# Optimization experiments

Measured on AMD Instinct MI355X. Metric: run time of the kernel, lower is better.

The kernel has to match this reference:

```python
import jax, jax.numpy as jnp
import numpy as np

K = 3
CHUNK = 1000  # query chunk size for KNN distance tiles
EPS = 1e-8
GRID = 256.0  # coordinate extent (coords / stride in the original)


def _knn3(queries, refs):
    """Brute-force KNN (K=3, squared L2) computed in chunks to bound memory.
    queries: [Q,3], refs: [M,3] -> (dist [Q,3], idx [Q,3] int32)."""
    ref_sq = jnp.sum(refs * refs, axis=-1)  # [M]

    def chunk_fn(q):  # q: [CHUNK,3]
        d = jnp.sum(q * q, -1)[:, None] - 2.0 * (q @ refs.T) + ref_sq[None, :]
        d = jnp.maximum(d, 0.0)  # guard tiny negatives from cancellation
        neg_d, idx = jax.lax.top_k(-d, K)
        return -neg_d, idx

    Q = queries.shape[0]
    qs = queries.reshape(Q // CHUNK, CHUNK, 3)
    dists, idxs = jax.lax.map(chunk_fn, qs)
    return dists.reshape(Q, K), idxs.reshape(Q, K)


def setup_inputs() -> dict:
    key = jax.random.key(0)
    k1, k2, k3, k4 = jax.random.split(key, 4)
    N1, N2, C = 20000, 20000, 8
    xyz1 = jax.random.uniform(k1, (N1, 3), dtype=jnp.float32) * GRID
    point1 = jax.random.normal(k2, (N1, C), dtype=jnp.float32)
    xyz2 = jax.random.uniform(k3, (N2, 3), dtype=jnp.float32) * GRID
    motion = jax.random.normal(k4, (N2, C, 3), dtype=jnp.float32)
    return {"xyz1": xyz1, "point1": point1, "xyz2": xyz2, "motion": motion}


def reference(xyz1, point1, xyz2, motion):
    # Motion-compensated inter prediction tail of inter_prediction.forward:
    # per-channel warp, KNN(K=3) into frame 1, inverse-distance interpolation.
    N2, C, _ = motion.shape
    # xyz2_ = xyz2.unsqueeze(2) + motion -> [N2*C, 3]
    xyz2_ = (xyz2[:, None, :] + motion).reshape(N2 * C, 3)
    dist, idx = _knn3(xyz2_, xyz1)                 # [N2*C,3]
    dist = dist + EPS
    dist = dist.reshape(N2, C, K)
    idx = idx.reshape(N2, C, K)
    weights = 1.0 / dist
    weights = weights / jnp.maximum(weights.sum(axis=2, keepdims=True), 3.0)
    # knn_point1[n,c,k] = point1[idx[n,c,k], c]  (per-channel gather)
    pt = point1.T                                   # [C, N1]
    knn_point1 = pt[jnp.arange(C)[None, :, None], idx]  # [N2,C,3]
    predicted_point2 = (weights * knn_point1).sum(axis=2)  # [N2,C]
    return predicted_point2
```

## Files before the change

### kernel.cpp

```cpp
#include <hip/hip_runtime.h>
#include <math.h>

#define KNN_EPS 1e-8f
#define GH 16.0f
#define GC 16
#define NCELLS (GC * GC * GC)
#define MARGIN 1.0f
#define CAP 384
#define CAPR 64
#define CAPQ 192


__device__ __forceinline__ int cell_coord(float v) {
    int c = (int)floorf(v * (1.0f / GH));
    return min(max(c, 0), GC - 1);
}

__global__ void fused_scatter_kernel(
    const float* __restrict__ xyz1, int n1,
    const float* __restrict__ xyz2,
    const float* __restrict__ motion, int n2, int C,
    int* __restrict__ counts, int* __restrict__ qcounts,
    float4* __restrict__ rbuck, float4* __restrict__ qbuck,
    float4* __restrict__ refspill, int* __restrict__ rsn,
    float4* __restrict__ qspill, int* __restrict__ qsn)
{
#pragma clang fp contract(off)
    int i = blockIdx.x * blockDim.x + threadIdx.x;
    if (i < n1) {
        float x = xyz1[3 * i + 0];
        float y = xyz1[3 * i + 1];
        float z = xyz1[3 * i + 2];
        int cid = (cell_coord(z) * GC + cell_coord(y)) * GC + cell_coord(x);
        int pos = atomicAdd(&counts[cid], 1);
        float4 v = make_float4(x, y, z, __int_as_float(i));
        if (pos < CAPR) rbuck[cid * CAPR + pos] = v;
        else { int sp = atomicAdd(rsn, 1); refspill[sp] = v; }
    }
    int nq = n2 * C;
    if (i < nq) {
        int n = i / C;
        float qx = xyz2[3 * n + 0] + motion[3 * i + 0];
        float qy = xyz2[3 * n + 1] + motion[3 * i + 1];
        float qz = xyz2[3 * n + 2] + motion[3 * i + 2];
        int cid = (cell_coord(qz) * GC + cell_coord(qy)) * GC + cell_coord(qx);
        int pos = atomicAdd(&qcounts[cid], 1);
        float4 v = make_float4(qx, qy, qz, __int_as_float(i));
        if (pos < CAPQ) qbuck[cid * CAPQ + pos] = v;
        else { int sp = atomicAdd(qsn, 1); qspill[sp] = v; }
    }
}

__device__ __forceinline__ void top3_insert_lex(float d, int j,
                                                float& bd0, float& bd1, float& bd2,
                                                int& bi0, int& bi1, int& bi2) {
    if (d < bd2 || (d == bd2 && j < bi2)) {
        if (d < bd1 || (d == bd1 && j < bi1)) {
            bd2 = bd1; bi2 = bi1;
            if (d < bd0 || (d == bd0 && j < bi0)) {
                bd1 = bd0; bi1 = bi0;
                bd0 = d;   bi0 = j;
            } else {
                bd1 = d;   bi1 = j;
            }
        } else {
            bd2 = d;       bi2 = j;
        }
    }
}

__device__ __forceinline__ void eval_candidate(
    float4 r, float qx, float qy, float qz, float qsq,
    float& bd0, float& bd1, float& bd2, int& bi0, int& bi1, int& bi2) {
    int ridx = __float_as_int(r.w);
    float rsq = r.x * r.x + r.y * r.y;
    rsq = rsq + r.z * r.z;
    float t = fmaf(qz, r.z, fmaf(qy, r.y, qx * r.x));
    float h = qsq + rsq;
    float d = fmaxf(fmaf(-2.0f, t, h), 0.0f);
    top3_insert_lex(d, ridx, bd0, bd1, bd2, bi0, bi1, bi2);
}

__device__ __forceinline__ float cert_radius(float qx, float qy, float qz,
                                             int icx, int icy, int icz, int rho) {
    float R = INFINITY;
    if (icx - rho > 0)      R = fminf(R, qx - (float)(icx - rho) * GH);
    if (icx + rho < GC - 1) R = fminf(R, (float)(icx + rho + 1) * GH - qx);
    if (icy - rho > 0)      R = fminf(R, qy - (float)(icy - rho) * GH);
    if (icy + rho < GC - 1) R = fminf(R, (float)(icy + rho + 1) * GH - qy);
    if (icz - rho > 0)      R = fminf(R, qz - (float)(icz - rho) * GH);
    if (icz + rho < GC - 1) R = fminf(R, (float)(icz + rho + 1) * GH - qz);
    return R;
}

__device__ __forceinline__ void epilogue_store(
    float bd0, float bd1, float bd2, int bi0, int bi1, int bi2,
    int qid, int C, const float* __restrict__ point1, float* __restrict__ out) {
#pragma clang fp contract(off)
    float dd0 = bd0 + KNN_EPS;
    float dd1 = bd1 + KNN_EPS;
    float dd2 = bd2 + KNN_EPS;
    float w0 = 1.0f / dd0;
    float w1 = 1.0f / dd1;
    float w2 = 1.0f / dd2;
    float s  = w0 + w1;
    s = s + w2;
    float m = fmaxf(s, 3.0f);
    w0 = w0 / m;
    w1 = w1 / m;
    w2 = w2 / m;
    const int c = qid - (qid / C) * C;
    float p0 = point1[bi0 * C + c];
    float p1 = point1[bi1 * C + c];
    float p2 = point1[bi2 * C + c];
    float acc = w0 * p0 + w1 * p1;
    acc = acc + w2 * p2;
    out[qid] = acc;
}

__device__ void ring_search(float qx, float qy, float qz, float qsq,
                            const float4* __restrict__ rbuck,
                            const int* __restrict__ counts, int rspn,
                            const float4* __restrict__ refspill,
                            float& bd0, float& bd1, float& bd2,
                            int& bi0, int& bi1, int& bi2) {
    const int icx = cell_coord(qx);
    const int icy = cell_coord(qy);
    const int icz = cell_coord(qz);
    for (int k = 0; k < rspn; ++k)
        eval_candidate(refspill[k], qx, qy, qz, qsq, bd0, bd1, bd2, bi0, bi1, bi2);
    for (int rho = 0; rho < GC; ++rho) {
        for (int dz = -rho; dz <= rho; ++dz) {
            int cz = icz + dz;
            if (cz < 0 || cz >= GC) continue;
            int adz = (dz < 0) ? -dz : dz;
            for (int dy = -rho; dy <= rho; ++dy) {
                int cy = icy + dy;
                if (cy < 0 || cy >= GC) continue;
                int ady = (dy < 0) ? -dy : dy;
                int step = (adz == rho || ady == rho || rho == 0) ? 1 : 2 * rho;
                for (int dx = -rho; dx <= rho; dx += step) {
                    int cx = icx + dx;
                    if (cx < 0 || cx >= GC) continue;
                    int cid = (cz * GC + cy) * GC + cx;
                    int e = min(counts[cid], CAPR);
                    for (int s = 0; s < e; ++s)
                        eval_candidate(rbuck[cid * CAPR + s], qx, qy, qz, qsq,
                                       bd0, bd1, bd2, bi0, bi1, bi2);
                }
            }
        }
        float Rr = cert_radius(qx, qy, qz, icx, icy, icz, rho);
        if (bd2 + MARGIN <= Rr * Rr) break;
    }
}

__global__ __launch_bounds__(128, 8) void knn_cell_kernel(
    const float4* __restrict__ rbuck,
    const int*   __restrict__ counts,
    const float4* __restrict__ refspill,
    const int*   __restrict__ rsn,
    const float4* __restrict__ qbuck,
    const int*   __restrict__ qcounts,
    const float* __restrict__ point1,
    float* __restrict__ out,
    int C)
{
#pragma clang fp contract(off)
    const int cell = blockIdx.x;
    const int qn = min(qcounts[cell], CAPQ);
    if (qn == 0) return;
    const int qbase = cell * CAPQ;

    const int tid = threadIdx.x;
    const int lane = tid & 63;
    const int wave = tid >> 6;

    const int icx = cell & (GC - 1);
    const int icy = (cell >> 4) & (GC - 1);
    const int icz = cell >> 8;

    __shared__ float4 cand[CAP];
    __shared__ int rcid[27], rlen[27], rofs[27], rst[27];
    __shared__ int total_s, ovf_s, rsn_s;
    __shared__ float pbd[64][3];
    __shared__ int   pbi[64][3];

    if (tid < 27) {
        int dz = tid / 9 - 1, dy = (tid / 3) % 3 - 1, dx = tid % 3 - 1;
        int cz = icz + dz, cy = icy + dy, cx = icx + dx;
        int ok = (cz >= 0 && cz < GC && cy >= 0 && cy < GC && cx >= 0 && cx < GC);
        int cid = ok ? (cz * GC + cy) * GC + cx : 0;
        rcid[tid] = cid;
        rlen[tid] = ok ? min(counts[cid], CAPR) : 0;
    }
    if (tid == 32) rsn_s = *rsn;
    __syncthreads();
    if (tid == 0) {
        int run = 0, ovf = 0;
        for (int r = 0; r < 27; ++r) {
            int len = rlen[r];
            int st = min(len, CAP - run);
            rofs[r] = run; rst[r] = st;
            run += st;
            if (st < len) ovf = 1;
        }
        total_s = run; ovf_s = ovf;
    }
    __syncthreads();

    const int total = total_s;
    const int ovf = ovf_s;
    const int rspn = rsn_s;

    for (int i = tid; i < total; i += 128) {
        int lo = 0, hi = 26;
        while (lo < hi) {
            int mid = (lo + hi + 1) >> 1;
            if (rofs[mid] <= i) lo = mid; else hi = mid - 1;
        }
        cand[i] = rbuck[rcid[lo] * CAPR + (i - rofs[lo])];
    }
    __syncthreads();

    const int half = total >> 1;
    const int k0 = wave ? half : 0;
    const int k1 = wave ? total : half;

    const int niter = (qn + 63) >> 6;
    for (int it = 0; it < niter; ++it) {
        const int qo = it * 64 + lane;
        const bool active = qo < qn;
        float4 Q = qbuck[qbase + (active ? qo : 0)];
        const float qx = Q.x, qy = Q.y, qz = Q.z;
        const int qid = __float_as_int(Q.w);
        float qsq = qx * qx + qy * qy;
        qsq = qsq + qz * qz;

        float bd0 = INFINITY, bd1 = INFINITY, bd2 = INFINITY;
        int   bi0 = 0,        bi1 = 0,        bi2 = 0;

        int k = k0;
        for (; k + 4 <= k1; k += 4) {
            float4 c0 = cand[k + 0];
            float4 c1 = cand[k + 1];
            float4 c2 = cand[k + 2];
            float4 c3 = cand[k + 3];
            eval_candidate(c0, qx, qy, qz, qsq, bd0, bd1, bd2, bi0, bi1, bi2);
            eval_candidate(c1, qx, qy, qz, qsq, bd0, bd1, bd2, bi0, bi1, bi2);
            eval_candidate(c2, qx, qy, qz, qsq, bd0, bd1, bd2, bi0, bi1, bi2);
            eval_candidate(c3, qx, qy, qz, qsq, bd0, bd1, bd2, bi0, bi1, bi2);
        }
        for (; k < k1; ++k)
            eval_candidate(cand[k], qx, qy, qz, qsq, bd0, bd1, bd2, bi0, bi1, bi2);

        if (wave == 1) {
            pbd[lane][0] = bd0; pbd[lane][1] = bd1; pbd[lane][2] = bd2;
            pbi[lane][0] = bi0; pbi[lane][1] = bi1; pbi[lane][2] = bi2;
        }
        __syncthreads();

        if (wave == 0) {
            for (int m = 0; m < 3; ++m) {
                float d = pbd[lane][m];
                if (d < INFINITY)
                    top3_insert_lex(d, pbi[lane][m], bd0, bd1, bd2, bi0, bi1, bi2);
            }
            for (int k2 = 0; k2 < rspn; ++k2)
                eval_candidate(refspill[k2], qx, qy, qz, qsq,
                               bd0, bd1, bd2, bi0, bi1, bi2);
            if (ovf) {
                for (int r = 0; r < 27; ++r)
                    for (int kk = rst[r]; kk < rlen[r]; ++kk)
                        eval_candidate(rbuck[rcid[r] * CAPR + kk], qx, qy, qz, qsq,
                                       bd0, bd1, bd2, bi0, bi1, bi2);
            }
            float R = cert_radius(qx, qy, qz, icx, icy, icz, 1);
            if (!(bd2 + MARGIN <= R * R)) {
                for (int rho = 2; rho < GC; ++rho) {
                    for (int dz = -rho; dz <= rho; ++dz) {
                        int cz = icz + dz;
                        if (cz < 0 || cz >= GC) continue;
                        int adz = (dz < 0) ? -dz : dz;
                        for (int dy = -rho; dy <= rho; ++dy) {
                            int cy = icy + dy;
                            if (cy < 0 || cy >= GC) continue;
                            int ady = (dy < 0) ? -dy : dy;
                            int step = (adz == rho || ady == rho) ? 1 : 2 * rho;
                            for (int dx = -rho; dx <= rho; dx += step) {
                                int cx = icx + dx;
                                if (cx < 0 || cx >= GC) continue;
                                int cid = (cz * GC + cy) * GC + cx;
                                int e = min(counts[cid], CAPR);
                                for (int s = 0; s < e; ++s)
                                    eval_candidate(rbuck[cid * CAPR + s],
                                                   qx, qy, qz, qsq,
                                                   bd0, bd1, bd2, bi0, bi1, bi2);
                            }
                        }
                    }
                    float Rr = cert_radius(qx, qy, qz, icx, icy, icz, rho);
                    if (bd2 + MARGIN <= Rr * Rr) break;
                }
            }

            if (active)
                epilogue_store(bd0, bd1, bd2, bi0, bi1, bi2, qid, C, point1, out);
        }
        if (it + 1 < niter) __syncthreads();
    }
}

__global__ __launch_bounds__(256) void qspill_kernel(
    const float4* __restrict__ qspill, const int* __restrict__ qsn,
    const float4* __restrict__ rbuck, const int* __restrict__ counts,
    const float4* __restrict__ refspill, const int* __restrict__ rsn,
    const float* __restrict__ point1, float* __restrict__ out, int C)
{
#pragma clang fp contract(off)
    const int nsp = *qsn;
    const int rspn = *rsn;
    for (int s = blockIdx.x * blockDim.x + threadIdx.x; s < nsp;
         s += gridDim.x * blockDim.x) {
        float4 Q = qspill[s];
        const float qx = Q.x, qy = Q.y, qz = Q.z;
        const int qid = __float_as_int(Q.w);
        float qsq = qx * qx + qy * qy;
        qsq = qsq + qz * qz;
        float bd0 = INFINITY, bd1 = INFINITY, bd2 = INFINITY;
        int   bi0 = 0,        bi1 = 0,        bi2 = 0;
        ring_search(qx, qy, qz, qsq, rbuck, counts, rspn, refspill,
                    bd0, bd1, bd2, bi0, bi1, bi2);
        epilogue_store(bd0, bd1, bd2, bi0, bi1, bi2, qid, C, point1, out);
    }
}

extern "C" void kernel_launch(void* const* d_in, const int* in_sizes, int n_in,
                              void* d_out, int out_size, void* d_ws, size_t ws_size,
                              hipStream_t stream) {
    const float* xyz1   = (const float*)d_in[0];
    const float* point1 = (const float*)d_in[1];
    const float* xyz2   = (const float*)d_in[2];
    const float* motion = (const float*)d_in[3];
    float* out = (float*)d_out;

    const int n1 = in_sizes[0] / 3;
    const int n2 = in_sizes[2] / 3;
    const int C  = in_sizes[1] / n1;
    const int nq = n2 * C;

    char* ws = (char*)d_ws;
    size_t off = 0;
    auto alloc = [&](size_t bytes) {
        char* p = ws + off;
        off = (off + bytes + 255) & ~(size_t)255;
        return p;
    };
    float4* rbuck    = (float4*)alloc((size_t)NCELLS * CAPR * 16);
    float4* qbuck    = (float4*)alloc((size_t)NCELLS * CAPQ * 16);
    float4* refspill = (float4*)alloc((size_t)n1 * 16);
    float4* qspill   = (float4*)alloc((size_t)nq * 16);
    int*    zero     = (int*)alloc((size_t)(2 * NCELLS + 2) * 4);
    int* counts  = zero;
    int* qcounts = zero + NCELLS;
    int* rsn     = zero + 2 * NCELLS;
    int* qsn     = zero + 2 * NCELLS + 1;

    const int nmax = (n1 > nq) ? n1 : nq;

    hipMemsetAsync(zero, 0, (size_t)(2 * NCELLS + 2) * 4, stream);
    fused_scatter_kernel<<<(nmax + 255) / 256, 256, 0, stream>>>(
        xyz1, n1, xyz2, motion, n2, C,
        counts, qcounts, rbuck, qbuck, refspill, rsn, qspill, qsn);
    knn_cell_kernel<<<NCELLS, 128, 0, stream>>>(
        rbuck, counts, refspill, rsn, qbuck, qcounts, point1, out, C);
    qspill_kernel<<<4, 256, 0, stream>>>(
        qspill, qsn, rbuck, counts, refspill, rsn, point1, out, C);
}
```

Measured before the change: 167.9 us.

## Drop LDS candidate staging; each wave handles own queries reading buckets directly

Removes the shared-memory staging of the 27-neighbour reference candidates and the two-wave split of the candidate list with its LDS merge and barriers. Instead each wave takes its own 64-query slice and streams the neighbour buckets straight from global memory (wave-uniform addresses, likely cache hits). This removes the syncthreads, the binary-search gather and the partial top-3 merge, and lets both waves run the spill and expansion paths in parallel. The cost is repeated global/L1 loads of the candidate data per wave instead of one LDS load, and serial per-wave work on the full 27-cell list.

```diff
diff --git a/kernel.cpp b/kernel.cpp
--- a/kernel.cpp
+++ b/kernel.cpp
@@ -6,7 +6,6 @@
 #define GC 16
 #define NCELLS (GC * GC * GC)
 #define MARGIN 1.0f
-#define CAP 384
 #define CAPR 64
 #define CAPQ 192
 
@@ -179,59 +178,12 @@
     const int icx = cell & (GC - 1);
     const int icy = (cell >> 4) & (GC - 1);
     const int icz = cell >> 8;
-
-    __shared__ float4 cand[CAP];
-    __shared__ int rcid[27], rlen[27], rofs[27], rst[27];
-    __shared__ int total_s, ovf_s, rsn_s;
-    __shared__ float pbd[64][3];
-    __shared__ int   pbi[64][3];
-
-    if (tid < 27) {
-        int dz = tid / 9 - 1, dy = (tid / 3) % 3 - 1, dx = tid % 3 - 1;
-        int cz = icz + dz, cy = icy + dy, cx = icx + dx;
-        int ok = (cz >= 0 && cz < GC && cy >= 0 && cy < GC && cx >= 0 && cx < GC);
-        int cid = ok ? (cz * GC + cy) * GC + cx : 0;
-        rcid[tid] = cid;
-        rlen[tid] = ok ? min(counts[cid], CAPR) : 0;
-    }
-    if (tid == 32) rsn_s = *rsn;
-    __syncthreads();
-    if (tid == 0) {
-        int run = 0, ovf = 0;
-        for (int r = 0; r < 27; ++r) {
-            int len = rlen[r];
-            int st = min(len, CAP - run);
-            rofs[r] = run; rst[r] = st;
-            run += st;
-            if (st < len) ovf = 1;
-        }
-        total_s = run; ovf_s = ovf;
-    }
-    __syncthreads();
-
-    const int total = total_s;
-    const int ovf = ovf_s;
-    const int rspn = rsn_s;
-
-    for (int i = tid; i < total; i += 128) {
-        int lo = 0, hi = 26;
-        while (lo < hi) {
-            int mid = (lo + hi + 1) >> 1;
-            if (rofs[mid] <= i) lo = mid; else hi = mid - 1;
-        }
-        cand[i] = rbuck[rcid[lo] * CAPR + (i - rofs[lo])];
-    }
-    __syncthreads();
-
-    const int half = total >> 1;
-    const int k0 = wave ? half : 0;
-    const int k1 = wave ? total : half;
-
-    const int niter = (qn + 63) >> 6;
-    for (int it = 0; it < niter; ++it) {
-        const int qo = it * 64 + lane;
+    const int rspn = *rsn;
+
+    for (int base = wave * 64; base < qn; base += 128) {
+        const int qo = base + lane;
         const bool active = qo < qn;
-        float4 Q = qbuck[qbase + (active ? qo : 0)];
+        float4 Q = qbuck[qbase + (active ? qo : base)];
         const float qx = Q.x, qy = Q.y, qz = Q.z;
         const int qid = __float_as_int(Q.w);
         float qsq = qx * qx + qy * qy;
@@ -240,74 +192,65 @@
         float bd0 = INFINITY, bd1 = INFINITY, bd2 = INFINITY;
         int   bi0 = 0,        bi1 = 0,        bi2 = 0;
 
-        int k = k0;
-        for (; k + 4 <= k1; k += 4) {
-            float4 c0 = cand[k + 0];
-            float4 c1 = cand[k + 1];
-            float4 c2 = cand[k + 2];
-            float4 c3 = cand[k + 3];
-            eval_candidate(c0, qx, qy, qz, qsq, bd0, bd1, bd2, bi0, bi1, bi2);
-            eval_candidate(c1, qx, qy, qz, qsq, bd0, bd1, bd2, bi0, bi1, bi2);
-            eval_candidate(c2, qx, qy, qz, qsq, bd0, bd1, bd2, bi0, bi1, bi2);
-            eval_candidate(c3, qx, qy, qz, qsq, bd0, bd1, bd2, bi0, bi1, bi2);
+        for (int r = 0; r < 27; ++r) {
+            const int dz = r / 9 - 1, dy = (r / 3) % 3 - 1, dx = r % 3 - 1;
+            const int cz = icz + dz, cy = icy + dy, cx = icx + dx;
+            if (cz < 0 || cz >= GC || cy < 0 || cy >= GC || cx < 0 || cx >= GC)
+                continue;
+            const int cid = (cz * GC + cy) * GC + cx;
+            const int e = min(counts[cid], CAPR);
+            const float4* __restrict__ cp = rbuck + (size_t)cid * CAPR;
+            int s = 0;
+            for (; s + 4 <= e; s += 4) {
+                float4 c0 = cp[s + 0];
+                float4 c1 = cp[s + 1];
+                float4 c2 = cp[s + 2];
+                float4 c3 = cp[s + 3];
+                eval_candidate(c0, qx, qy, qz, qsq, bd0, bd1, bd2, bi0, bi1, bi2);
+                eval_candidate(c1, qx, qy, qz, qsq, bd0, bd1, bd2, bi0, bi1, bi2);
+                eval_candidate(c2, qx, qy, qz, qsq, bd0, bd1, bd2, bi0, bi1, bi2);
+                eval_candidate(c3, qx, qy, qz, qsq, bd0, bd1, bd2, bi0, bi1, bi2);
+            }
+            for (; s < e; ++s)
+                eval_candidate(cp[s], qx, qy, qz, qsq,
+                               bd0, bd1, bd2, bi0, bi1, bi2);
         }
-        for (; k < k1; ++k)
-            eval_candidate(cand[k], qx, qy, qz, qsq, bd0, bd1, bd2, bi0, bi1, bi2);
-
-        if (wave == 1) {
-            pbd[lane][0] = bd0; pbd[lane][1] = bd1; pbd[lane][2] = bd2;
-            pbi[lane][0] = bi0; pbi[lane][1] = bi1; pbi[lane][2] = bi2;
-        }
-        __syncthreads();
-
-        if (wave == 0) {
-            for (int m = 0; m < 3; ++m) {
-                float d = pbd[lane][m];
-                if (d < INFINITY)
-                    top3_insert_lex(d, pbi[lane][m], bd0, bd1, bd2, bi0, bi1, bi2);
-            }
-            for (int k2 = 0; k2 < rspn; ++k2)
-                eval_candidate(refspill[k2], qx, qy, qz, qsq,
-                               bd0, bd1, bd2, bi0, bi1, bi2);
-            if (ovf) {
-                for (int r = 0; r < 27; ++r)
-                    for (int kk = rst[r]; kk < rlen[r]; ++kk)
-                        eval_candidate(rbuck[rcid[r] * CAPR + kk], qx, qy, qz, qsq,
-                                       bd0, bd1, bd2, bi0, bi1, bi2);
-            }
-            float R = cert_radius(qx, qy, qz, icx, icy, icz, 1);
-            if (!(bd2 + MARGIN <= R * R)) {
-                for (int rho = 2; rho < GC; ++rho) {
-                    for (int dz = -rho; dz <= rho; ++dz) {
-                        int cz = icz + dz;
-                        if (cz < 0 || cz >= GC) continue;
-                        int adz = (dz < 0) ? -dz : dz;
-                        for (int dy = -rho; dy <= rho; ++dy) {
-                            int cy = icy + dy;
-                            if (cy < 0 || cy >= GC) continue;
-                            int ady = (dy < 0) ? -dy : dy;
-                            int step = (adz == rho || ady == rho) ? 1 : 2 * rho;
-                            for (int dx = -rho; dx <= rho; dx += step) {
-                                int cx = icx + dx;
-                                if (cx < 0 || cx >= GC) continue;
-                                int cid = (cz * GC + cy) * GC + cx;
-                                int e = min(counts[cid], CAPR);
-                                for (int s = 0; s < e; ++s)
-                                    eval_candidate(rbuck[cid * CAPR + s],
-                                                   qx, qy, qz, qsq,
-                                                   bd0, bd1, bd2, bi0, bi1, bi2);
-                            }
+
+        for (int k = 0; k < rspn; ++k)
+            eval_candidate(refspill[k], qx, qy, qz, qsq,
+                           bd0, bd1, bd2, bi0, bi1, bi2);
+
+        float R = cert_radius(qx, qy, qz, icx, icy, icz, 1);
+        if (!(bd2 + MARGIN <= R * R)) {
+            for (int rho = 2; rho < GC; ++rho) {
+                for (int dz = -rho; dz <= rho; ++dz) {
+                    int cz = icz + dz;
+                    if (cz < 0 || cz >= GC) continue;
+                    int adz = (dz < 0) ? -dz : dz;
+                    for (int dy = -rho; dy <= rho; ++dy) {
+                        int cy = icy + dy;
+                        if (cy < 0 || cy >= GC) continue;
+                        int ady = (dy < 0) ? -dy : dy;
+                        int step = (adz == rho || ady == rho) ? 1 : 2 * rho;
+                        for (int dx = -rho; dx <= rho; dx += step) {
+                            int cx = icx + dx;
+                            if (cx < 0 || cx >= GC) continue;
+                            int cid = (cz * GC + cy) * GC + cx;
+                            int e = min(counts[cid], CAPR);
+                            for (int s = 0; s < e; ++s)
+                                eval_candidate(rbuck[cid * CAPR + s],
+                                               qx, qy, qz, qsq,
+                                               bd0, bd1, bd2, bi0, bi1, bi2);
                         }
                     }
-                    float Rr = cert_radius(qx, qy, qz, icx, icy, icz, rho);
-                    if (bd2 + MARGIN <= Rr * Rr) break;
                 }
+                float Rr = cert_radius(qx, qy, qz, icx, icy, icz, rho);
+                if (bd2 + MARGIN <= Rr * Rr) break;
             }
-
-            if (active)
-                epilogue_store(bd0, bd1, bd2, bi0, bi1, bi2, qid, C, point1, out);
         }
-        if (it + 1 < niter) __syncthreads();
+
+        if (active)
+            epilogue_store(bd0, bd1, bd2, bi0, bi1, bi2, qid, C, point1, out);
     }
 }
 
```

Result: slower. 171.4 us (+2.1%).
